# Kernel optimization log

Measured on AMD Instinct MI355X. Metric: run time of the kernel, lower is better.

## Reference

```python
import jax, jax.numpy as jnp
import numpy as np

N = 100000          # n_nodes
E = 3200000         # n_edges (avg degree 32)
IN_FEATS = 256
H = 128             # h_feats
N_HOPS = 4


def setup_inputs() -> dict:
    key = jax.random.key(0)
    ks = jax.random.split(key, 8)
    edge_index = jax.random.randint(ks[0], (2, E), 0, N, dtype=jnp.int32)
    features = jax.random.normal(ks[1], (N, IN_FEATS), dtype=jnp.float32)
    # input block: Linear(in_feats, h_feats)
    W0 = jax.random.normal(ks[2], (IN_FEATS, H), dtype=jnp.float32) / np.sqrt(IN_FEATS)
    b0 = jnp.zeros((H,), jnp.float32)
    # per-hop GCNConv bias (weight=False because RN=='attentive')
    biases = jnp.zeros((N_HOPS, H), jnp.float32)
    # per-hop attention gate: Linear(2*h_feats, 1) + tanh
    Watt = jax.random.normal(ks[3], (N_HOPS, 2 * H), dtype=jnp.float32) / np.sqrt(2 * H)
    batt = jnp.zeros((N_HOPS,), jnp.float32)
    return {"edge_index": edge_index, "features": features,
            "W0": W0, "b0": b0, "biases": biases, "Watt": Watt, "batt": batt}


def _gcn_agg(x, src, dst):
    # symmetric GCN normalization with self-loops: D^-1/2 (A+I) D^-1/2 @ x
    deg = jnp.zeros((N,), x.dtype).at[dst].add(1.0) + 1.0  # +1 for self-loop
    dinv = jax.lax.rsqrt(deg)
    w = dinv[src] * dinv[dst]                               # [E]
    out = jnp.zeros((N, x.shape[1]), x.dtype).at[dst].add(x[src] * w[:, None])
    return out + x * (dinv * dinv)[:, None]                 # self-loop term


def reference(edge_index, features, W0, b0, biases, Watt, batt):
    src, dst = edge_index[0], edge_index[1]
    # hop-0 input block (dropout=0, norm=Identity)
    h = jax.nn.relu(features @ W0 + b0)                     # [N, H]
    for i in range(N_HOPS):
        # GCNConv with weight=False: aggregation + bias + act
        h_k = jax.nn.relu(_gcn_agg(h, src, dst) + biases[i])
        # attentive hop combination: a = tanh(Linear([h_k, h]))
        a = jnp.tanh(jnp.concatenate([h_k, h], axis=-1) @ Watt[i] + batt[i])[:, None]
        h = a * h_k + (1.0 - a) * h
    return h
```

## Files before the change

### kernel.cpp

```cpp
#include <hip/hip_runtime.h>
#include <hip/hip_fp16.h>
#include <math.h>

#define N_NODES 100000
#define N_EDGES 3200000
#define IN_F 256
#define H 128
#define N_HOPS 4
#define SCAN_B 256
#define BSH 5
#define NBUCK ((N_NODES + 31) >> BSH)

typedef _Float16 half8_t __attribute__((ext_vector_type(8)));
typedef float f32x4 __attribute__((ext_vector_type(4)));


__global__ void deg_kernel(const int* __restrict__ dst, int* __restrict__ deg) {
    int e = blockIdx.x * blockDim.x + threadIdx.x;
    if (e < N_EDGES) atomicAdd(&deg[dst[e]], 1);
}

__global__ void dinv_kernel(const int* __restrict__ deg, float* __restrict__ dinv) {
    int n = blockIdx.x * blockDim.x + threadIdx.x;
    if (n < N_NODES) dinv[n] = rsqrtf((float)deg[n] + 1.0f);
}

__global__ void scan_p1(const int* __restrict__ deg, int* __restrict__ bsum) {
    __shared__ int s[SCAN_B];
    int n = blockIdx.x * SCAN_B + threadIdx.x;
    s[threadIdx.x] = (n < N_NODES) ? deg[n] : 0;
    __syncthreads();
    for (int off = SCAN_B / 2; off; off >>= 1) {
        if (threadIdx.x < off) s[threadIdx.x] += s[threadIdx.x + off];
        __syncthreads();
    }
    if (threadIdx.x == 0) bsum[blockIdx.x] = s[0];
}

__global__ void scan_p2(int* __restrict__ bsum, int nb) {
    __shared__ int s[512];
    int t = threadIdx.x;
    int v0 = (t < nb) ? bsum[t] : 0;
    s[t] = v0;
    __syncthreads();
    for (int off = 1; off < 512; off <<= 1) {
        int v = (t >= off) ? s[t - off] : 0;
        __syncthreads();
        s[t] += v;
        __syncthreads();
    }
    if (t < nb) bsum[t] = s[t] - v0;
}

__global__ void scan_p3(const int* __restrict__ deg, const int* __restrict__ boff,
                        int* __restrict__ rowptr) {
    __shared__ int s[SCAN_B];
    int n = blockIdx.x * SCAN_B + threadIdx.x;
    int v = (n < N_NODES) ? deg[n] : 0;
    s[threadIdx.x] = v;
    __syncthreads();
    for (int off = 1; off < SCAN_B; off <<= 1) {
        int t = (threadIdx.x >= off) ? s[threadIdx.x - off] : 0;
        __syncthreads();
        s[threadIdx.x] += t;
        __syncthreads();
    }
    int incl = s[threadIdx.x];
    int excl = incl - v;
    if (n < N_NODES) rowptr[n] = boff[blockIdx.x] + excl;
    if (n == N_NODES - 1) rowptr[N_NODES] = boff[blockIdx.x] + incl;
}

__global__ void bucket_p1(const int* __restrict__ src, const int* __restrict__ dst,
                          const int* __restrict__ rowptr, int* __restrict__ bcur,
                          uint2* __restrict__ tmp) {
    int e = blockIdx.x * blockDim.x + threadIdx.x;
    if (e >= N_EDGES) return;
    int s = src[e], d = dst[e];
    int b = d >> BSH;
    int pos = rowptr[b << BSH] + atomicAdd(&bcur[b], 1);
    tmp[pos] = make_uint2((unsigned)s, (unsigned)d);
}

__global__ void scatter2(const uint2* __restrict__ tmp, const float* __restrict__ dinv,
                         const int* __restrict__ rowptr, int* __restrict__ cursor,
                         uint2* __restrict__ edges) {
    int e = blockIdx.x * blockDim.x + threadIdx.x;
    if (e >= N_EDGES) return;
    uint2 ev = tmp[e];
    int s = (int)ev.x, d = (int)ev.y;
    int pos = rowptr[d] + atomicAdd(&cursor[d], 1);
    edges[pos] = make_uint2(ev.x, __float_as_uint(dinv[s] * dinv[d]));
}

__global__ void w16_kernel(const float* __restrict__ W0, _Float16* __restrict__ W16t) {
    int t = blockIdx.x * 256 + threadIdx.x;
    if (t < H * IN_F) {
        int n = t >> 8;
        int k = t & 255;
        W16t[(size_t)n * IN_F + k] = (_Float16)W0[(size_t)k * H + n];
    }
}

__global__ __launch_bounds__(256) void mfma_gemm(const float* __restrict__ X,
                                                 const _Float16* __restrict__ W16t,
                                                 const float* __restrict__ b0,
                                                 __half* __restrict__ h16) {
    __shared__ _Float16 Al[128 * 64];
    __shared__ _Float16 Bl[128 * 64];
    int tid = threadIdx.x;
    int wv = tid >> 6, ln = tid & 63;
    size_t node0 = (size_t)blockIdx.x * 128;

    f32x4 acc[2][8];
#pragma unroll
    for (int mi = 0; mi < 2; ++mi)
#pragma unroll
        for (int ni = 0; ni < 8; ++ni) acc[mi][ni] = (f32x4)(0.f);

    int arow = tid >> 1;
    int koff = (tid & 1) * 32;
    bool arow_ok = (node0 + (size_t)arow) < N_NODES;

    for (int k0 = 0; k0 < IN_F; k0 += 64) {
#pragma unroll
        for (int j = 0; j < 4; ++j) {
            float4 u0 = make_float4(0.f, 0.f, 0.f, 0.f), u1 = u0;
            if (arow_ok) {
                const float4* xp = (const float4*)(X + (node0 + (size_t)arow) * IN_F + k0 + koff + j * 8);
                u0 = xp[0]; u1 = xp[1];
            }
            half8_t hv;
            hv[0] = (_Float16)u0.x; hv[1] = (_Float16)u0.y;
            hv[2] = (_Float16)u0.z; hv[3] = (_Float16)u0.w;
            hv[4] = (_Float16)u1.x; hv[5] = (_Float16)u1.y;
            hv[6] = (_Float16)u1.z; hv[7] = (_Float16)u1.w;
            int unit = (koff >> 3) + j;
            *(half8_t*)&Al[arow * 64 + ((unit ^ (arow & 7)) << 3)] = hv;
        }
        {
            const half8_t* wp = (const half8_t*)(W16t + (size_t)arow * IN_F + k0 + koff);
#pragma unroll
            for (int j = 0; j < 4; ++j) {
                half8_t hv = wp[j];
                int unit = (koff >> 3) + j;
                *(half8_t*)&Bl[arow * 64 + ((unit ^ (arow & 7)) << 3)] = hv;
            }
        }
        __syncthreads();
#pragma unroll
        for (int ks = 0; ks < 2; ++ks) {
            int lk = ks * 4 + (ln >> 4);
            int l15 = ln & 15;
            half8_t a[2], b[8];
#pragma unroll
            for (int mi = 0; mi < 2; ++mi) {
                int row = wv * 32 + mi * 16 + l15;
                a[mi] = *(half8_t*)&Al[row * 64 + ((lk ^ (row & 7)) << 3)];
            }
#pragma unroll
            for (int ni = 0; ni < 8; ++ni) {
                int col = ni * 16 + l15;
                b[ni] = *(half8_t*)&Bl[col * 64 + ((lk ^ (col & 7)) << 3)];
            }
#pragma unroll
            for (int mi = 0; mi < 2; ++mi)
#pragma unroll
                for (int ni = 0; ni < 8; ++ni)
                    acc[mi][ni] = __builtin_amdgcn_mfma_f32_16x16x32_f16(a[mi], b[ni], acc[mi][ni], 0, 0, 0);
        }
        __syncthreads();
    }

    int cgrp = ln >> 4, ccol = ln & 15;
#pragma unroll
    for (int mi = 0; mi < 2; ++mi)
#pragma unroll
        for (int ni = 0; ni < 8; ++ni) {
            int col = ni * 16 + ccol;
            float bb = b0[col];
#pragma unroll
            for (int r = 0; r < 4; ++r) {
                size_t node = node0 + (size_t)(wv * 32 + mi * 16 + cgrp * 4 + r);
                if (node < N_NODES) {
                    float v = acc[mi][ni][r] + bb;
                    h16[node * H + col] = __float2half(v > 0.f ? v : 0.f);
                }
            }
        }
}

__global__ __launch_bounds__(256) void hop_kernel(const __half* __restrict__ h_in,
                                                  __half* __restrict__ h16_out,
                                                  float* __restrict__ out32,
                                                  const int* __restrict__ rowptr,
                                                  const uint2* __restrict__ edges,
                                                  const float* __restrict__ dinv,
                                                  const float* __restrict__ bias,
                                                  const float* __restrict__ Wa,
                                                  const float* __restrict__ batt) {
    int wid = threadIdx.x >> 6;
    int lane = threadIdx.x & 63;
    int n = blockIdx.x * 4 + wid;
    if (n >= N_NODES) return;

    float2 hn = __half22float2(((const __half2*)(h_in + (size_t)n * H))[lane]);
    float dd = dinv[n];
    dd = dd * dd;
    float accx = hn.x * dd, accy = hn.y * dd;

    int e0 = rowptr[n], e1 = rowptr[n + 1];
    for (int base = e0; base < e1; base += 64) {
        int cnt = e1 - base;
        if (cnt > 64) cnt = 64;
        int sv = 0;
        float wv = 0.f;
        if (lane < cnt) {
            uint2 ev = edges[base + lane];
            sv = (int)ev.x;
            wv = __uint_as_float(ev.y);
        }
        int j = 0;
        for (; j + 3 < cnt; j += 4) {
            int s0 = __shfl(sv, j + 0), s1 = __shfl(sv, j + 1);
            int s2 = __shfl(sv, j + 2), s3 = __shfl(sv, j + 3);
            float w0 = __shfl(wv, j + 0), w1 = __shfl(wv, j + 1);
            float w2 = __shfl(wv, j + 2), w3 = __shfl(wv, j + 3);
            float2 g0 = __half22float2(((const __half2*)(h_in + (size_t)s0 * H))[lane]);
            float2 g1 = __half22float2(((const __half2*)(h_in + (size_t)s1 * H))[lane]);
            float2 g2 = __half22float2(((const __half2*)(h_in + (size_t)s2 * H))[lane]);
            float2 g3 = __half22float2(((const __half2*)(h_in + (size_t)s3 * H))[lane]);
            accx += w0 * g0.x + w1 * g1.x + w2 * g2.x + w3 * g3.x;
            accy += w0 * g0.y + w1 * g1.y + w2 * g2.y + w3 * g3.y;
        }
        for (; j < cnt; ++j) {
            int sj = __shfl(sv, j);
            float wj = __shfl(wv, j);
            float2 g = __half22float2(((const __half2*)(h_in + (size_t)sj * H))[lane]);
            accx += wj * g.x;
            accy += wj * g.y;
        }
    }

    float hkx = accx + bias[2 * lane];     hkx = hkx > 0.f ? hkx : 0.f;
    float hky = accy + bias[2 * lane + 1]; hky = hky > 0.f ? hky : 0.f;

    float p = hkx * Wa[2 * lane] + hky * Wa[2 * lane + 1]
            + hn.x * Wa[H + 2 * lane] + hn.y * Wa[H + 2 * lane + 1];
#pragma unroll
    for (int off = 32; off; off >>= 1) p += __shfl_xor(p, off);
    float a = tanhf(p + batt[0]);

    float ox = a * hkx + (1.f - a) * hn.x;
    float oy = a * hky + (1.f - a) * hn.y;
    if (out32) {
        ((float2*)(out32 + (size_t)n * H))[lane] = make_float2(ox, oy);
    } else {
        ((__half2*)(h16_out + (size_t)n * H))[lane] = __floats2half2_rn(ox, oy);
    }
}


extern "C" void kernel_launch(void* const* d_in, const int* in_sizes, int n_in,
                              void* d_out, int out_size, void* d_ws, size_t ws_size,
                              hipStream_t stream) {
    const int* edge_index = (const int*)d_in[0];
    const int* src = edge_index;
    const int* dst = edge_index + N_EDGES;
    const float* features = (const float*)d_in[1];
    const float* W0 = (const float*)d_in[2];
    const float* b0 = (const float*)d_in[3];
    const float* biases = (const float*)d_in[4];
    const float* Watt = (const float*)d_in[5];
    const float* batt = (const float*)d_in[6];
    float* out = (float*)d_out;

    size_t off = 0;
    char* base = (char*)d_ws;
    auto carve = [&](size_t bytes) -> void* {
        void* q = base + off;
        off += (bytes + 255) & ~(size_t)255;
        return q;
    };
    int* deg = (int*)carve((size_t)N_NODES * 4);
    float* dinv = (float*)carve((size_t)N_NODES * 4);
    int* rowptr = (int*)carve((size_t)(N_NODES + 1) * 4);
    int* cursor = (int*)carve((size_t)N_NODES * 4);
    int* bcur = (int*)carve((size_t)NBUCK * 4);
    int* bsum = (int*)carve(4096);
    uint2* edges = (uint2*)carve((size_t)N_EDGES * 8);
    _Float16* W16t = (_Float16*)carve((size_t)H * IN_F * 2);
    __half* h16A = (__half*)carve((size_t)N_NODES * H * 2);
    __half* h16B = (__half*)carve((size_t)N_NODES * H * 2);
    uint2* tmp = (uint2*)h16B;

    hipMemsetAsync(deg, 0, (size_t)N_NODES * 4, stream);
    hipMemsetAsync(cursor, 0, (size_t)N_NODES * 4, stream);
    hipMemsetAsync(bcur, 0, (size_t)NBUCK * 4, stream);

    int eb = (N_EDGES + 255) / 256;
    int nbN = (N_NODES + 255) / 256;
    deg_kernel<<<eb, 256, 0, stream>>>(dst, deg);
    dinv_kernel<<<nbN, 256, 0, stream>>>(deg, dinv);
    scan_p1<<<nbN, SCAN_B, 0, stream>>>(deg, bsum);
    scan_p2<<<1, 512, 0, stream>>>(bsum, nbN);
    scan_p3<<<nbN, SCAN_B, 0, stream>>>(deg, bsum, rowptr);
    bucket_p1<<<eb, 256, 0, stream>>>(src, dst, rowptr, bcur, tmp);
    scatter2<<<eb, 256, 0, stream>>>(tmp, dinv, rowptr, cursor, edges);

    w16_kernel<<<(H * IN_F + 255) / 256, 256, 0, stream>>>(W0, W16t);
    mfma_gemm<<<(N_NODES + 127) / 128, 256, 0, stream>>>(features, W16t, b0, h16A);

    __half* hin = h16A;
    __half* hout = h16B;
    for (int i = 0; i < N_HOPS; ++i) {
        bool last = (i == N_HOPS - 1);
        hop_kernel<<<(N_NODES + 3) / 4, 256, 0, stream>>>(
            hin, hout, last ? out : nullptr, rowptr, edges, dinv,
            biases + (size_t)i * H, Watt + (size_t)i * 2 * H, batt + i);
        __half* t = hin; hin = hout; hout = t;
    }
}
```

Measured before the change: 1.198 ms.

## Build CSR with shared-memory two-level counting sort and drop per-edge weights

Replaces the seven-kernel CSR build (global degree atomics, three-pass scan, two global-atomic scatters) with a two-level counting sort. Edges are first binned into 512-node windows using per-block LDS histograms and staging buffers, then each window is sorted by destination in LDS; that second pass also produces rowptr and dinv. The edge array now holds only the 4-byte source index instead of a (src, weight) pair. The hop kernel rebuilds the weight by gathering dinv[src] and applies dinv[dst] once after accumulating, which halves the edge-stream bytes but adds a random dinv gather per edge.

```diff
diff --git a/kernel.cpp b/kernel.cpp
--- a/kernel.cpp
+++ b/kernel.cpp
@@ -7,90 +7,126 @@
 #define IN_F 256
 #define H 128
 #define N_HOPS 4
-#define SCAN_B 256
-#define BSH 5
-#define NBUCK ((N_NODES + 31) >> BSH)
+#define BWIN 512
+#define NB_C ((N_NODES + BWIN - 1) / BWIN)
+#define CH 8192
 
 typedef _Float16 half8_t __attribute__((ext_vector_type(8)));
 typedef float f32x4 __attribute__((ext_vector_type(4)));
 
-
-__global__ void deg_kernel(const int* __restrict__ dst, int* __restrict__ deg) {
-    int e = blockIdx.x * blockDim.x + threadIdx.x;
-    if (e < N_EDGES) atomicAdd(&deg[dst[e]], 1);
-}
-
-__global__ void dinv_kernel(const int* __restrict__ deg, float* __restrict__ dinv) {
-    int n = blockIdx.x * blockDim.x + threadIdx.x;
-    if (n < N_NODES) dinv[n] = rsqrtf((float)deg[n] + 1.0f);
-}
-
-__global__ void scan_p1(const int* __restrict__ deg, int* __restrict__ bsum) {
-    __shared__ int s[SCAN_B];
-    int n = blockIdx.x * SCAN_B + threadIdx.x;
-    s[threadIdx.x] = (n < N_NODES) ? deg[n] : 0;
-    __syncthreads();
-    for (int off = SCAN_B / 2; off; off >>= 1) {
-        if (threadIdx.x < off) s[threadIdx.x] += s[threadIdx.x + off];
-        __syncthreads();
-    }
-    if (threadIdx.x == 0) bsum[blockIdx.x] = s[0];
-}
-
-__global__ void scan_p2(int* __restrict__ bsum, int nb) {
-    __shared__ int s[512];
+__global__ __launch_bounds__(256) void bcount_kernel(const int* __restrict__ dst,
+                                                     int* __restrict__ bcount) {
+    __shared__ int hist[NB_C];
+    int tid = threadIdx.x;
+    for (int b = tid; b < NB_C; b += 256) hist[b] = 0;
+    __syncthreads();
+    int e0 = blockIdx.x * CH, e1 = min(e0 + CH, N_EDGES);
+    for (int e = e0 + tid; e < e1; e += 256) atomicAdd(&hist[dst[e] >> 9], 1);
+    __syncthreads();
+    for (int b = tid; b < NB_C; b += 256)
+        if (hist[b]) atomicAdd(&bcount[b], hist[b]);
+}
+
+__global__ void bscan_kernel(const int* __restrict__ bcount, int* __restrict__ bbase) {
+    __shared__ int s[256];
     int t = threadIdx.x;
-    int v0 = (t < nb) ? bsum[t] : 0;
-    s[t] = v0;
-    __syncthreads();
-    for (int off = 1; off < 512; off <<= 1) {
-        int v = (t >= off) ? s[t - off] : 0;
-        __syncthreads();
-        s[t] += v;
-        __syncthreads();
-    }
-    if (t < nb) bsum[t] = s[t] - v0;
-}
-
-__global__ void scan_p3(const int* __restrict__ deg, const int* __restrict__ boff,
-                        int* __restrict__ rowptr) {
-    __shared__ int s[SCAN_B];
-    int n = blockIdx.x * SCAN_B + threadIdx.x;
-    int v = (n < N_NODES) ? deg[n] : 0;
-    s[threadIdx.x] = v;
-    __syncthreads();
-    for (int off = 1; off < SCAN_B; off <<= 1) {
-        int t = (threadIdx.x >= off) ? s[threadIdx.x - off] : 0;
-        __syncthreads();
-        s[threadIdx.x] += t;
-        __syncthreads();
-    }
-    int incl = s[threadIdx.x];
-    int excl = incl - v;
-    if (n < N_NODES) rowptr[n] = boff[blockIdx.x] + excl;
-    if (n == N_NODES - 1) rowptr[N_NODES] = boff[blockIdx.x] + incl;
-}
-
-__global__ void bucket_p1(const int* __restrict__ src, const int* __restrict__ dst,
-                          const int* __restrict__ rowptr, int* __restrict__ bcur,
-                          uint2* __restrict__ tmp) {
-    int e = blockIdx.x * blockDim.x + threadIdx.x;
-    if (e >= N_EDGES) return;
-    int s = src[e], d = dst[e];
-    int b = d >> BSH;
-    int pos = rowptr[b << BSH] + atomicAdd(&bcur[b], 1);
-    tmp[pos] = make_uint2((unsigned)s, (unsigned)d);
-}
-
-__global__ void scatter2(const uint2* __restrict__ tmp, const float* __restrict__ dinv,
-                         const int* __restrict__ rowptr, int* __restrict__ cursor,
-                         uint2* __restrict__ edges) {
-    int e = blockIdx.x * blockDim.x + threadIdx.x;
-    if (e >= N_EDGES) return;
-    uint2 ev = tmp[e];
-    int s = (int)ev.x, d = (int)ev.y;
-    int pos = rowptr[d] + atomicAdd(&cursor[d], 1);
-    edges[pos] = make_uint2(ev.x, __float_as_uint(dinv[s] * dinv[d]));
+    int v = (t < NB_C) ? bcount[t] : 0;
+    s[t] = v;
+    __syncthreads();
+    for (int o = 1; o < 256; o <<= 1) {
+        int x = (t >= o) ? s[t - o] : 0;
+        __syncthreads();
+        s[t] += x;
+        __syncthreads();
+    }
+    if (t < NB_C) bbase[t] = s[t] - v;
+    if (t == 0) bbase[NB_C] = N_EDGES;
+}
+
+__global__ __launch_bounds__(256) void bin_kernel(const int* __restrict__ src,
+                                                  const int* __restrict__ dst,
+                                                  const int* __restrict__ bbase,
+                                                  int* __restrict__ gcur,
+                                                  uint2* __restrict__ tmp) {
+    __shared__ uint2 binbuf[CH];
+    __shared__ int hist[NB_C], cur[NB_C], off[NB_C];
+    __shared__ int s[256];
+    int tid = threadIdx.x;
+    int e0 = blockIdx.x * CH, e1 = min(e0 + CH, N_EDGES);
+
+    for (int b = tid; b < NB_C; b += 256) hist[b] = 0;
+    __syncthreads();
+    for (int e = e0 + tid; e < e1; e += 256) atomicAdd(&hist[dst[e] >> 9], 1);
+    __syncthreads();
+    int v = (tid < NB_C) ? hist[tid] : 0;
+    s[tid] = v;
+    __syncthreads();
+    for (int o = 1; o < 256; o <<= 1) {
+        int x = (tid >= o) ? s[tid - o] : 0;
+        __syncthreads();
+        s[tid] += x;
+        __syncthreads();
+    }
+    if (tid < NB_C) { off[tid] = s[tid] - v; cur[tid] = s[tid] - v; }
+    __syncthreads();
+    for (int e = e0 + tid; e < e1; e += 256) {
+        int d = dst[e];
+        int b = d >> 9;
+        int p = atomicAdd(&cur[b], 1);
+        binbuf[p] = make_uint2((unsigned)src[e], (unsigned)d);
+    }
+    __syncthreads();
+    int wid = tid >> 6, lane = tid & 63;
+    for (int b = wid; b < NB_C; b += 4) {
+        int cnt = hist[b];
+        if (cnt == 0) continue;
+        int g;
+        if (lane == 0) g = atomicAdd(&gcur[b], cnt);
+        g = __shfl(g, 0);
+        uint2* dp = tmp + (size_t)bbase[b] + g;
+        const uint2* sp = binbuf + off[b];
+        for (int i = lane; i < cnt; i += 64) dp[i] = sp[i];
+    }
+}
+
+__global__ __launch_bounds__(512) void sort_kernel(const uint2* __restrict__ tmp,
+                                                   const int* __restrict__ bbase,
+                                                   int* __restrict__ rowptr,
+                                                   float* __restrict__ dinv,
+                                                   int* __restrict__ es) {
+    __shared__ int hist[BWIN], sc[BWIN], cur[BWIN];
+    int tid = threadIdx.x;
+    int nb0 = blockIdx.x * BWIN;
+    int eb = bbase[blockIdx.x];
+    int ecnt = bbase[blockIdx.x + 1] - eb;
+
+    hist[tid] = 0;
+    __syncthreads();
+    for (int i = tid; i < ecnt; i += 512) atomicAdd(&hist[(int)tmp[eb + i].y - nb0], 1);
+    __syncthreads();
+    int v = hist[tid];
+    sc[tid] = v;
+    __syncthreads();
+    for (int o = 1; o < 512; o <<= 1) {
+        int x = (tid >= o) ? sc[tid - o] : 0;
+        __syncthreads();
+        sc[tid] += x;
+        __syncthreads();
+    }
+    int excl = sc[tid] - v;
+    cur[tid] = excl;
+    int node = nb0 + tid;
+    if (node < N_NODES) {
+        rowptr[node] = eb + excl;
+        dinv[node] = rsqrtf((float)v + 1.0f);
+    }
+    if (node == 0) rowptr[N_NODES] = N_EDGES;
+    __syncthreads();
+    for (int i = tid; i < ecnt; i += 512) {
+        uint2 ev = tmp[eb + i];
+        int p = atomicAdd(&cur[(int)ev.y - nb0], 1);
+        es[eb + p] = (int)ev.x;
+    }
 }
 
 __global__ void w16_kernel(const float* __restrict__ W0, _Float16* __restrict__ W16t) {
@@ -194,7 +230,7 @@
                                                   __half* __restrict__ h16_out,
                                                   float* __restrict__ out32,
                                                   const int* __restrict__ rowptr,
-                                                  const uint2* __restrict__ edges,
+                                                  const int* __restrict__ es,
                                                   const float* __restrict__ dinv,
                                                   const float* __restrict__ bias,
                                                   const float* __restrict__ Wa,
@@ -205,9 +241,8 @@
     if (n >= N_NODES) return;
 
     float2 hn = __half22float2(((const __half2*)(h_in + (size_t)n * H))[lane]);
-    float dd = dinv[n];
-    dd = dd * dd;
-    float accx = hn.x * dd, accy = hn.y * dd;
+    float dn = dinv[n];
+    float accx = hn.x * dn, accy = hn.y * dn;
 
     int e0 = rowptr[n], e1 = rowptr[n + 1];
     for (int base = e0; base < e1; base += 64) {
@@ -216,9 +251,8 @@
         int sv = 0;
         float wv = 0.f;
         if (lane < cnt) {
-            uint2 ev = edges[base + lane];
-            sv = (int)ev.x;
-            wv = __uint_as_float(ev.y);
+            sv = es[base + lane];
+            wv = dinv[sv];
         }
         int j = 0;
         for (; j + 3 < cnt; j += 4) {
@@ -242,8 +276,8 @@
         }
     }
 
-    float hkx = accx + bias[2 * lane];     hkx = hkx > 0.f ? hkx : 0.f;
-    float hky = accy + bias[2 * lane + 1]; hky = hky > 0.f ? hky : 0.f;
+    float hkx = accx * dn + bias[2 * lane];     hkx = hkx > 0.f ? hkx : 0.f;
+    float hky = accy * dn + bias[2 * lane + 1]; hky = hky > 0.f ? hky : 0.f;
 
     float p = hkx * Wa[2 * lane] + hky * Wa[2 * lane + 1]
             + hn.x * Wa[H + 2 * lane] + hn.y * Wa[H + 2 * lane + 1];
@@ -282,31 +316,25 @@
         off += (bytes + 255) & ~(size_t)255;
         return q;
     };
-    int* deg = (int*)carve((size_t)N_NODES * 4);
     float* dinv = (float*)carve((size_t)N_NODES * 4);
     int* rowptr = (int*)carve((size_t)(N_NODES + 1) * 4);
-    int* cursor = (int*)carve((size_t)N_NODES * 4);
-    int* bcur = (int*)carve((size_t)NBUCK * 4);
-    int* bsum = (int*)carve(4096);
-    uint2* edges = (uint2*)carve((size_t)N_EDGES * 8);
+    int* bcount = (int*)carve((size_t)NB_C * 4);
+    int* bbase = (int*)carve((size_t)(NB_C + 1) * 4);
+    int* gcur = (int*)carve((size_t)NB_C * 4);
+    int* es = (int*)carve((size_t)N_EDGES * 4);
     _Float16* W16t = (_Float16*)carve((size_t)H * IN_F * 2);
     __half* h16A = (__half*)carve((size_t)N_NODES * H * 2);
     __half* h16B = (__half*)carve((size_t)N_NODES * H * 2);
-    uint2* tmp = (uint2*)h16B;
-
-    hipMemsetAsync(deg, 0, (size_t)N_NODES * 4, stream);
-    hipMemsetAsync(cursor, 0, (size_t)N_NODES * 4, stream);
-    hipMemsetAsync(bcur, 0, (size_t)NBUCK * 4, stream);
-
-    int eb = (N_EDGES + 255) / 256;
-    int nbN = (N_NODES + 255) / 256;
-    deg_kernel<<<eb, 256, 0, stream>>>(dst, deg);
-    dinv_kernel<<<nbN, 256, 0, stream>>>(deg, dinv);
-    scan_p1<<<nbN, SCAN_B, 0, stream>>>(deg, bsum);
-    scan_p2<<<1, 512, 0, stream>>>(bsum, nbN);
-    scan_p3<<<nbN, SCAN_B, 0, stream>>>(deg, bsum, rowptr);
-    bucket_p1<<<eb, 256, 0, stream>>>(src, dst, rowptr, bcur, tmp);
-    scatter2<<<eb, 256, 0, stream>>>(tmp, dinv, rowptr, cursor, edges);
+    uint2* tmp = (uint2*)carve((size_t)N_EDGES * 8);
+
+    hipMemsetAsync(bcount, 0, (size_t)NB_C * 4, stream);
+    hipMemsetAsync(gcur, 0, (size_t)NB_C * 4, stream);
+
+    int ebCH = (N_EDGES + CH - 1) / CH;
+    bcount_kernel<<<ebCH, 256, 0, stream>>>(dst, bcount);
+    bscan_kernel<<<1, 256, 0, stream>>>(bcount, bbase);
+    bin_kernel<<<ebCH, 256, 0, stream>>>(src, dst, bbase, gcur, tmp);
+    sort_kernel<<<NB_C, 512, 0, stream>>>(tmp, bbase, rowptr, dinv, es);
 
     w16_kernel<<<(H * IN_F + 255) / 256, 256, 0, stream>>>(W0, W16t);
     mfma_gemm<<<(N_NODES + 127) / 128, 256, 0, stream>>>(features, W16t, b0, h16A);
@@ -316,7 +344,7 @@
     for (int i = 0; i < N_HOPS; ++i) {
         bool last = (i == N_HOPS - 1);
         hop_kernel<<<(N_NODES + 3) / 4, 256, 0, stream>>>(
-            hin, hout, last ? out : nullptr, rowptr, edges, dinv,
+            hin, hout, last ? out : nullptr, rowptr, es, dinv,
             biases + (size_t)i * H, Watt + (size_t)i * 2 * H, batt + i);
         __half* t = hin; hin = hout; hout = t;
     }
```

Result: faster. 1.049 ms (-12.4%).
